# Kernel tuning notes

Hardware: AMD Instinct MI355X
Metric: run time of the kernel (lower is better)

The kernel has to match this reference:

```python
import jax, jax.numpy as jnp
import numpy as np

N = 100000   # nodes
E = 220000   # directed edges (each branch)
H = 128      # hidden_dim
OUT = 1      # output_dim
G = 4096     # num graphs in batch
PE = 5       # laplacian eigenvector PE dims
VOCAB = 28   # atom types


def gcn_conv(x, src, dst, W, b, n):
    # PyG GCNConv: x' = D^-1/2 (A + I) D^-1/2 (X W) + b
    h = x @ W
    deg = jax.ops.segment_sum(jnp.ones(src.shape[0], x.dtype), dst, num_segments=n) + 1.0
    dinv = jax.lax.rsqrt(deg)
    coef = dinv[src] * dinv[dst]                                    # [E]
    agg = jax.ops.segment_sum(h[src] * coef[:, None], dst, num_segments=n)
    agg = agg + h * (dinv * dinv)[:, None]                          # self-loop term
    return agg + b


def gcn2(x, edge_index, W1, b1, W2, b2, n):
    # PyG GCN model, num_layers=2: conv -> relu -> conv
    src, dst = edge_index[0], edge_index[1]
    h = jax.nn.relu(gcn_conv(x, src, dst, W1, b1, n))
    return gcn_conv(h, src, dst, W2, b2, n)


def setup_inputs() -> dict:
    key = jax.random.key(0)
    ks = jax.random.split(key, 16)
    s = 0.1
    return {
        "node_tokens": jax.random.randint(ks[0], (N, 1), 0, VOCAB),
        "pe": jax.random.normal(ks[1], (N, PE), jnp.float32),
        "edge_index": jax.random.randint(ks[2], (2, E), 0, N),
        "vr_edge_index": jax.random.randint(ks[3], (2, E), 0, N),
        "batch": jnp.sort(jax.random.randint(ks[4], (N,), 0, G)),
        "embed_table": jax.random.normal(ks[5], (VOCAB, H), jnp.float32) * s,
        "Wt": jax.random.normal(ks[6], (PE, H), jnp.float32) * s,
        "bt": jnp.zeros((H,), jnp.float32),
        "W1": jax.random.normal(ks[7], (H, H), jnp.float32) * s,
        "b1": jnp.zeros((H,), jnp.float32),
        "W2": jax.random.normal(ks[8], (H, OUT), jnp.float32) * s,
        "b2": jnp.zeros((OUT,), jnp.float32),
        "Wv1": jax.random.normal(ks[9], (H, H), jnp.float32) * s,
        "bv1": jnp.zeros((H,), jnp.float32),
        "Wv2": jax.random.normal(ks[10], (H, OUT), jnp.float32) * s,
        "bv2": jnp.zeros((OUT,), jnp.float32),
    }


def reference(node_tokens, pe, edge_index, vr_edge_index, batch, embed_table,
              Wt, bt, W1, b1, W2, b2, Wv1, bv1, Wv2, bv2):
    # embed_x(data.x.long()).squeeze(1) + lin_trans(pe)
    x = embed_table[node_tokens[:, 0]] + (pe @ Wt + bt)             # [N, H]
    x1 = gcn2(x, edge_index, W1, b1, W2, b2, N)                     # [N, OUT]
    xv = gcn2(x, vr_edge_index, Wv1, bv1, Wv2, bv2, N)              # [N, OUT]
    x1 = x1 + xv
    y_hat = jax.ops.segment_sum(x1, batch, num_segments=G)          # [G, OUT]
    y_hat = jnp.squeeze(y_hat, axis=-1)                             # [G]
    return (y_hat, x)
```

## Files before the change

### kernel.cpp

```cpp
#include <hip/hip_runtime.h>

#define NN 100000
#define NE 220000
#define HD 128
#define NG 4096
#define NPE 5
#define NB_SCAN ((NN + 255) / 256)
#define NBX4 ((NN * HD / 4) / 256)
#define NT16 (NN / 16)
#define NBGEMM 1024
#define NBW 128
#define NBE2 14
#define NBD ((2 * NE + 255) / 256)

typedef unsigned int uint;
typedef unsigned short ushort;
typedef __attribute__((ext_vector_type(8))) short bf16x8;
typedef __attribute__((ext_vector_type(4))) float f32x4;

__device__ __forceinline__ float bf2f(uint u16) {
    return __uint_as_float(u16 << 16);
}
__device__ __forceinline__ ushort f2bf(float f) {
    uint u = __float_as_uint(f);
    u += 0x7fffu + ((u >> 16) & 1u);
    return (ushort)(u >> 16);
}

__global__ void k_prep0(const float* __restrict__ W1, const float* __restrict__ Wv1,
                        const float* __restrict__ embed, const float* __restrict__ bt,
                        ushort* __restrict__ Wcat, float* __restrict__ emb2,
                        const int* __restrict__ ei, const int* __restrict__ vei,
                        int* __restrict__ cnt, int* __restrict__ rank) {
    int b = blockIdx.x;
    if (b < NBW) {
        int t = b * 256 + threadIdx.x;
        int f = t >> 7, k = t & 127;
        const float* W = (f < HD) ? W1 : Wv1;
        Wcat[t] = f2bf(W[k * HD + (f & 127)]);
    } else if (b < NBW + NBE2) {
        int t = (b - NBW) * 256 + threadIdx.x;
        if (t < 28 * 128) emb2[t] = embed[t] + bt[t & 127];
    } else {
        int t = (b - NBW - NBE2) * 256 + threadIdx.x;
        if (t < 2 * NE) {
            int br = t >= NE;
            int e = t - br * NE;
            const int* S = br ? vei : ei;
            rank[t] = atomicAdd(&cnt[br * NN + S[NE + e]], 1);
        }
    }
}

__global__ void k_front_scan1(const int* __restrict__ tok, const float* __restrict__ pe,
                              const float* __restrict__ emb2,
                              const float* __restrict__ Wtr,
                              float* __restrict__ x, ushort* __restrict__ xb,
                              const int* __restrict__ cnt, int* __restrict__ off,
                              int* __restrict__ bsum, float* __restrict__ dinv,
                              float* __restrict__ y) {
    __shared__ int s[256];
    int b = blockIdx.x;
    if (b < 2 * NB_SCAN) {
        int tid = threadIdx.x;
        int gid = b * 256 + tid;
        if (gid < NG) y[gid] = 0.f;
        int br = b / NB_SCAN;
        int blk = b % NB_SCAN;
        int i = blk * 256 + tid;
        int v = (i < NN) ? cnt[br * NN + i] : 0;
        if (i < NN) dinv[br * NN + i] = rsqrtf((float)v + 1.0f);
        s[tid] = v;
        __syncthreads();
        for (int d = 1; d < 256; d <<= 1) {
            int t = (tid >= d) ? s[tid - d] : 0;
            __syncthreads();
            s[tid] += t;
            __syncthreads();
        }
        if (i < NN) off[br * NN + i] = s[tid] - v;
        if (tid == 255) bsum[br * 512 + blk] = s[255];
    } else {
        int idx = (b - 2 * NB_SCAN) * 256 + threadIdx.x;
        int n = idx >> 5, q = idx & 31;
        int t = tok[n];
        float4 acc = ((const float4*)(emb2 + (size_t)t * HD))[q];
        const float* pen = pe + n * NPE;
#pragma unroll
        for (int k = 0; k < NPE; ++k) {
            float p = pen[k];
            float4 wv = ((const float4*)(Wtr + k * HD))[q];
            acc.x += p * wv.x; acc.y += p * wv.y;
            acc.z += p * wv.z; acc.w += p * wv.w;
        }
        ((float4*)x)[idx] = acc;
        uint2 pk;
        pk.x = (uint)f2bf(acc.x) | ((uint)f2bf(acc.y) << 16);
        pk.y = (uint)f2bf(acc.z) | ((uint)f2bf(acc.w) << 16);
        ((uint2*)xb)[idx] = pk;
    }
}

__global__ __launch_bounds__(256) void k_gemm_scan3(
        const ushort* __restrict__ xb, const ushort* __restrict__ Wt,
        ushort* __restrict__ H,
        const int* __restrict__ off, const int* __restrict__ bsum,
        const int* __restrict__ cnt, int2* __restrict__ off2) {
    __shared__ int s[256];
    int b = blockIdx.x;
    if (b < 2 * NB_SCAN) {
        int br = b / NB_SCAN;
        int blk = b % NB_SCAN;
        int tid = threadIdx.x;
        int v = 0;
        if (tid < blk) v = bsum[br * 512 + tid];
        if (tid + 256 < blk) v += bsum[br * 512 + tid + 256];
        s[tid] = v;
#pragma unroll
        for (int d = 128; d > 0; d >>= 1) {
            __syncthreads();
            if (tid < d) s[tid] += s[tid + d];
        }
        __syncthreads();
        int pre = s[0];
        int i = blk * 256 + tid;
        if (i < NN) {
            int o = off[br * NN + i] + pre;
            int2 pr;
            pr.x = o;
            pr.y = o + cnt[br * NN + i];
            off2[br * NN + i] = pr;
        }
    } else {
        int w = threadIdx.x >> 6;
        int lane = threadIdx.x & 63;
        int m = lane & 15, quad = lane >> 4;
        const ushort* Wbase = Wt + ((size_t)(w * 4) * 16 + m) * 128 + quad * 8;
        bf16x8 wf[4][4];
#pragma unroll
        for (int j = 0; j < 4; ++j)
#pragma unroll
            for (int kc = 0; kc < 4; ++kc)
                wf[j][kc] = *(const bf16x8*)(Wbase + (size_t)j * 16 * 128 + kc * 32);

        for (int t = b - 2 * NB_SCAN; t < NT16; t += NBGEMM) {
            int n = t * 16 + m;
            const ushort* Arow = xb + (size_t)n * HD + quad * 8;
            bf16x8 xf[4];
#pragma unroll
            for (int kc = 0; kc < 4; ++kc)
                xf[kc] = *(const bf16x8*)(Arow + kc * 32);
            f32x4 acc[4] = {};
#pragma unroll
            for (int j = 0; j < 4; ++j)
#pragma unroll
                for (int kc = 0; kc < 4; ++kc)
                    acc[j] = __builtin_amdgcn_mfma_f32_16x16x32_bf16(wf[j][kc], xf[kc],
                                                                     acc[j], 0, 0, 0);
#pragma unroll
            for (int j = 0; j < 4; ++j) {
                f32x4 a = acc[j];
                uint2 pk;
                pk.x = (uint)f2bf(a[0]) | ((uint)f2bf(a[1]) << 16);
                pk.y = (uint)f2bf(a[2]) | ((uint)f2bf(a[3]) << 16);
                *(uint2*)&H[(size_t)n * 256 + (w * 4 + j) * 16 + quad * 4] = pk;
            }
        }
    }
}

__global__ void k_scatter(const int* __restrict__ ei, const int* __restrict__ vei,
                          const int* __restrict__ rank, const float* __restrict__ dinv,
                          const int2* __restrict__ off2, int2* __restrict__ ent) {
    int t = blockIdx.x * blockDim.x + threadIdx.x;
    if (t >= 2 * NE) return;
    int br = t >= NE;
    int e = t - br * NE;
    const int* S = br ? vei : ei;
    int s = S[e], d = S[NE + e];
    int pos = off2[br * NN + d].x + rank[t];
    int2 rec;
    rec.x = s;
    rec.y = __float_as_int(dinv[br * NN + s] * dinv[br * NN + d]);
    ent[br * NE + pos] = rec;
}

__global__ void k_gather_ep(const ushort* __restrict__ H, const float* __restrict__ dinv,
                            const int2* __restrict__ off2,
                            const int2* __restrict__ ent,
                            const float* __restrict__ b1, const float* __restrict__ bv1,
                            const float* __restrict__ W2, const float* __restrict__ Wv2,
                            float* __restrict__ z) {
    int wid = threadIdx.x >> 6;
    int lane = threadIdx.x & 63;
    int half = lane >> 5;
    int l = lane & 31;
    int task = blockIdx.x * 8 + wid * 2 + half;
    int br = task >= NN;
    int n = task - br * NN;

    const int2* en = ent + br * NE;
    size_t hoff = (size_t)br * 128;

    int2 pr = off2[br * NN + n];
    int p0 = pr.x, p1 = pr.y;

    float dv = dinv[br * NN + n];
    uint2 u = *(const uint2*)(H + (size_t)n * 256 + hoff + l * 4);
    float c = dv * dv;
    float a0 = bf2f(u.x & 0xffffu) * c, a1 = bf2f(u.x >> 16) * c;
    float a2 = bf2f(u.y & 0xffffu) * c, a3 = bf2f(u.y >> 16) * c;

    for (int p = p0; p < p1; p += 4) {
        int2 e0 = en[p], e1 = en[p + 1], e2 = en[p + 2], e3 = en[p + 3];
        int s0 = e0.x;
        int s1 = (p + 1 < p1) ? e1.x : n;
        int s2 = (p + 2 < p1) ? e2.x : n;
        int s3 = (p + 3 < p1) ? e3.x : n;
        float c0 = __int_as_float(e0.y);
        float c1 = (p + 1 < p1) ? __int_as_float(e1.y) : 0.f;
        float c2 = (p + 2 < p1) ? __int_as_float(e2.y) : 0.f;
        float c3 = (p + 3 < p1) ? __int_as_float(e3.y) : 0.f;
        uint2 v0 = *(const uint2*)(H + (size_t)s0 * 256 + hoff + l * 4);
        uint2 v1 = *(const uint2*)(H + (size_t)s1 * 256 + hoff + l * 4);
        uint2 v2 = *(const uint2*)(H + (size_t)s2 * 256 + hoff + l * 4);
        uint2 v3 = *(const uint2*)(H + (size_t)s3 * 256 + hoff + l * 4);
        a0 += bf2f(v0.x & 0xffffu) * c0; a1 += bf2f(v0.x >> 16) * c0;
        a2 += bf2f(v0.y & 0xffffu) * c0; a3 += bf2f(v0.y >> 16) * c0;
        a0 += bf2f(v1.x & 0xffffu) * c1; a1 += bf2f(v1.x >> 16) * c1;
        a2 += bf2f(v1.y & 0xffffu) * c1; a3 += bf2f(v1.y >> 16) * c1;
        a0 += bf2f(v2.x & 0xffffu) * c2; a1 += bf2f(v2.x >> 16) * c2;
        a2 += bf2f(v2.y & 0xffffu) * c2; a3 += bf2f(v2.y >> 16) * c2;
        a0 += bf2f(v3.x & 0xffffu) * c3; a1 += bf2f(v3.x >> 16) * c3;
        a2 += bf2f(v3.y & 0xffffu) * c3; a3 += bf2f(v3.y >> 16) * c3;
    }

    const float* bb = br ? bv1 : b1;
    const float* ww = br ? Wv2 : W2;
    float4 b4 = *(const float4*)&bb[l * 4];
    float4 w4 = *(const float4*)&ww[l * 4];
    float part = fmaxf(a0 + b4.x, 0.f) * w4.x + fmaxf(a1 + b4.y, 0.f) * w4.y
               + fmaxf(a2 + b4.z, 0.f) * w4.z + fmaxf(a3 + b4.w, 0.f) * w4.w;
#pragma unroll
    for (int o = 16; o > 0; o >>= 1) part += __shfl_down(part, o, 32);
    if (l == 0) z[br * NN + n] = part;
}

__global__ void k_final2(const float* __restrict__ z, const float* __restrict__ dinv,
                         const int2* __restrict__ off2,
                         const int2* __restrict__ ent,
                         const float* __restrict__ b2, const float* __restrict__ bv2,
                         const int* __restrict__ batch, float* __restrict__ y) {
    __shared__ float ybuf[256];
    __shared__ int gbase_s;
    int br = blockIdx.x >= NB_SCAN;
    int nb = blockIdx.x - br * NB_SCAN;
    int tid = threadIdx.x;
    ybuf[tid] = 0.f;
    if (tid == 0) gbase_s = batch[nb * 256];
    __syncthreads();
    int gbase = gbase_s;
    int n = nb * 256 + tid;
    if (n < NN) {
        const int2* en = ent + br * NE;
        float dv = dinv[br * NN + n];
        float acc = z[br * NN + n] * dv * dv;
        int2 pr = off2[br * NN + n];
        int p1 = pr.y;
        for (int p = pr.x; p < p1; p += 4) {
            int2 e0 = en[p], e1 = en[p + 1], e2 = en[p + 2], e3 = en[p + 3];
            int s0 = e0.x;
            int s1 = (p + 1 < p1) ? e1.x : n;
            int s2 = (p + 2 < p1) ? e2.x : n;
            int s3 = (p + 3 < p1) ? e3.x : n;
            float c0 = __int_as_float(e0.y);
            float c1 = (p + 1 < p1) ? __int_as_float(e1.y) : 0.f;
            float c2 = (p + 2 < p1) ? __int_as_float(e2.y) : 0.f;
            float c3 = (p + 3 < p1) ? __int_as_float(e3.y) : 0.f;
            acc += c0 * z[br * NN + s0] + c1 * z[br * NN + s1]
                 + c2 * z[br * NN + s2] + c3 * z[br * NN + s3];
        }
        acc += br ? bv2[0] : b2[0];
        int gi = batch[n] - gbase;
        if (gi < 256) atomicAdd(&ybuf[gi], acc);
        else atomicAdd(&y[batch[n]], acc);
    }
    __syncthreads();
    float v = ybuf[tid];
    if (v != 0.f) atomicAdd(&y[gbase + tid], v);
}

extern "C" void kernel_launch(void* const* d_in, const int* in_sizes, int n_in,
                              void* d_out, int out_size, void* d_ws, size_t ws_size,
                              hipStream_t stream) {
    const int*   tok   = (const int*)d_in[0];
    const float* pe    = (const float*)d_in[1];
    const int*   ei    = (const int*)d_in[2];
    const int*   vei   = (const int*)d_in[3];
    const int*   batch = (const int*)d_in[4];
    const float* embed = (const float*)d_in[5];
    const float* Wtr   = (const float*)d_in[6];
    const float* bt    = (const float*)d_in[7];
    const float* W1    = (const float*)d_in[8];
    const float* b1    = (const float*)d_in[9];
    const float* W2    = (const float*)d_in[10];
    const float* b2    = (const float*)d_in[11];
    const float* Wv1   = (const float*)d_in[12];
    const float* bv1   = (const float*)d_in[13];
    const float* Wv2   = (const float*)d_in[14];
    const float* bv2   = (const float*)d_in[15];

    float* y = (float*)d_out;
    float* x = y + NG;

    char* w = (char*)d_ws;
    ushort* xb   = (ushort*)w;               w += (size_t)NN * HD * 2;
    ushort* H    = (ushort*)w;               w += (size_t)NN * 256 * 2;
    ushort* Wcat = (ushort*)w;               w += 256 * 128 * 2;
    float*  emb2 = (float*)w;                w += 28 * 128 * 4;
    float*  dinv = (float*)w;                w += 2 * NN * 4;
    float*  z    = (float*)w;                w += 2 * NN * 4;
    int*    cnt  = (int*)w;                  w += 2 * NN * 4;
    int*    off  = (int*)w;                  w += 2 * NN * 4;
    int*    rank = (int*)w;                  w += (size_t)2 * NE * 4;
    int2*   off2 = (int2*)w;                 w += (size_t)2 * NN * 8;
    int2*   ent  = (int2*)w;                 w += (size_t)(2 * NE + 8) * 8;
    int*    bsum = (int*)w;                  w += 2 * 512 * 4;

    hipMemsetAsync(cnt, 0, 2 * NN * sizeof(int), stream);

    k_prep0<<<NBW + NBE2 + NBD, 256, 0, stream>>>(W1, Wv1, embed, bt, Wcat, emb2,
                                                  ei, vei, cnt, rank);
    k_front_scan1<<<2 * NB_SCAN + NBX4, 256, 0, stream>>>(tok, pe, emb2, Wtr, x, xb,
                                                          cnt, off, bsum, dinv, y);
    k_gemm_scan3<<<2 * NB_SCAN + NBGEMM, 256, 0, stream>>>(xb, Wcat, H,
                                                           off, bsum, cnt, off2);
    k_scatter<<<NBD, 256, 0, stream>>>(ei, vei, rank, dinv, off2, ent);
    k_gather_ep<<<2 * NN / 8, 256, 0, stream>>>(H, dinv, off2, ent,
                                                b1, bv1, W2, Wv2, z);
    k_final2<<<2 * NB_SCAN, 256, 0, stream>>>(z, dinv, off2, ent,
                                              b2, bv2, batch, y);
}
```

Measured before the change: 222.1 us.

## Add fixed 4-slot per-node edge table to remove dependent offset load in gathers

Adds a padded per-node array that holds the first four incoming edges (source, coefficient) and is filled during the scatter. The gather and final kernels can then load these slots directly, indexed by node id, at the same time as the offset pair, rather than waiting for the CSR offset before fetching edges. The goal is to shorten the dependent-load chain for the typical low-degree node (about 2.2 edges per node). In exchange it enlarges the memset, adds an extra write per edge and 6.4 MB of workspace, and the CSR loop still handles edges beyond the fourth. Empty slots are zeroed, so their coefficient is zero and their index points at node 0.

```diff
diff --git a/kernel.cpp b/kernel.cpp
--- a/kernel.cpp
+++ b/kernel.cpp
@@ -171,23 +171,28 @@
 
 __global__ void k_scatter(const int* __restrict__ ei, const int* __restrict__ vei,
                           const int* __restrict__ rank, const float* __restrict__ dinv,
-                          const int2* __restrict__ off2, int2* __restrict__ ent) {
+                          const int2* __restrict__ off2, int2* __restrict__ ent,
+                          int2* __restrict__ ent8) {
     int t = blockIdx.x * blockDim.x + threadIdx.x;
     if (t >= 2 * NE) return;
     int br = t >= NE;
     int e = t - br * NE;
     const int* S = br ? vei : ei;
     int s = S[e], d = S[NE + e];
-    int pos = off2[br * NN + d].x + rank[t];
+    int rk = rank[t];
+    int base = br * NN + d;
+    int pos = off2[base].x + rk;
     int2 rec;
     rec.x = s;
     rec.y = __float_as_int(dinv[br * NN + s] * dinv[br * NN + d]);
     ent[br * NE + pos] = rec;
+    if (rk < 4) ent8[base * 4 + rk] = rec;
 }
 
 __global__ void k_gather_ep(const ushort* __restrict__ H, const float* __restrict__ dinv,
                             const int2* __restrict__ off2,
                             const int2* __restrict__ ent,
+                            const int4* __restrict__ ent8,
                             const float* __restrict__ b1, const float* __restrict__ bv1,
                             const float* __restrict__ W2, const float* __restrict__ Wv2,
                             float* __restrict__ z) {
@@ -201,17 +206,38 @@
 
     const int2* en = ent + br * NE;
     size_t hoff = (size_t)br * 128;
-
-    int2 pr = off2[br * NN + n];
-    int p0 = pr.x, p1 = pr.y;
-
-    float dv = dinv[br * NN + n];
+    int base = br * NN + n;
+
+    int4 e01 = ent8[base * 2];
+    int4 e23 = ent8[base * 2 + 1];
+    int2 pr = off2[base];
+    float dv = dinv[base];
     uint2 u = *(const uint2*)(H + (size_t)n * 256 + hoff + l * 4);
+
     float c = dv * dv;
     float a0 = bf2f(u.x & 0xffffu) * c, a1 = bf2f(u.x >> 16) * c;
     float a2 = bf2f(u.y & 0xffffu) * c, a3 = bf2f(u.y >> 16) * c;
 
-    for (int p = p0; p < p1; p += 4) {
+    {
+        int s0 = e01.x, s1 = e01.z, s2 = e23.x, s3 = e23.z;
+        float c0 = __int_as_float(e01.y), c1 = __int_as_float(e01.w);
+        float c2 = __int_as_float(e23.y), c3 = __int_as_float(e23.w);
+        uint2 v0 = *(const uint2*)(H + (size_t)s0 * 256 + hoff + l * 4);
+        uint2 v1 = *(const uint2*)(H + (size_t)s1 * 256 + hoff + l * 4);
+        uint2 v2 = *(const uint2*)(H + (size_t)s2 * 256 + hoff + l * 4);
+        uint2 v3 = *(const uint2*)(H + (size_t)s3 * 256 + hoff + l * 4);
+        a0 += bf2f(v0.x & 0xffffu) * c0; a1 += bf2f(v0.x >> 16) * c0;
+        a2 += bf2f(v0.y & 0xffffu) * c0; a3 += bf2f(v0.y >> 16) * c0;
+        a0 += bf2f(v1.x & 0xffffu) * c1; a1 += bf2f(v1.x >> 16) * c1;
+        a2 += bf2f(v1.y & 0xffffu) * c1; a3 += bf2f(v1.y >> 16) * c1;
+        a0 += bf2f(v2.x & 0xffffu) * c2; a1 += bf2f(v2.x >> 16) * c2;
+        a2 += bf2f(v2.y & 0xffffu) * c2; a3 += bf2f(v2.y >> 16) * c2;
+        a0 += bf2f(v3.x & 0xffffu) * c3; a1 += bf2f(v3.x >> 16) * c3;
+        a2 += bf2f(v3.y & 0xffffu) * c3; a3 += bf2f(v3.y >> 16) * c3;
+    }
+
+    int p1 = pr.y;
+    for (int p = pr.x + 4; p < p1; p += 4) {
         int2 e0 = en[p], e1 = en[p + 1], e2 = en[p + 2], e3 = en[p + 3];
         int s0 = e0.x;
         int s1 = (p + 1 < p1) ? e1.x : n;
@@ -249,6 +275,7 @@
 __global__ void k_final2(const float* __restrict__ z, const float* __restrict__ dinv,
                          const int2* __restrict__ off2,
                          const int2* __restrict__ ent,
+                         const int4* __restrict__ ent8,
                          const float* __restrict__ b2, const float* __restrict__ bv2,
                          const int* __restrict__ batch, float* __restrict__ y) {
     __shared__ float ybuf[256];
@@ -263,11 +290,20 @@
     int n = nb * 256 + tid;
     if (n < NN) {
         const int2* en = ent + br * NE;
-        float dv = dinv[br * NN + n];
-        float acc = z[br * NN + n] * dv * dv;
-        int2 pr = off2[br * NN + n];
+        int base = br * NN + n;
+        int4 e01 = ent8[base * 2];
+        int4 e23 = ent8[base * 2 + 1];
+        int2 pr = off2[base];
+        float dv = dinv[base];
+        float acc = z[base] * dv * dv;
+        {
+            float c0 = __int_as_float(e01.y), c1 = __int_as_float(e01.w);
+            float c2 = __int_as_float(e23.y), c3 = __int_as_float(e23.w);
+            acc += c0 * z[br * NN + e01.x] + c1 * z[br * NN + e01.z]
+                 + c2 * z[br * NN + e23.x] + c3 * z[br * NN + e23.z];
+        }
         int p1 = pr.y;
-        for (int p = pr.x; p < p1; p += 4) {
+        for (int p = pr.x + 4; p < p1; p += 4) {
             int2 e0 = en[p], e1 = en[p + 1], e2 = en[p + 2], e3 = en[p + 3];
             int s0 = e0.x;
             int s1 = (p + 1 < p1) ? e1.x : n;
@@ -321,13 +357,14 @@
     float*  dinv = (float*)w;                w += 2 * NN * 4;
     float*  z    = (float*)w;                w += 2 * NN * 4;
     int*    cnt  = (int*)w;                  w += 2 * NN * 4;
+    int2*   ent8 = (int2*)w;                 w += (size_t)2 * NN * 4 * 8;
     int*    off  = (int*)w;                  w += 2 * NN * 4;
     int*    rank = (int*)w;                  w += (size_t)2 * NE * 4;
     int2*   off2 = (int2*)w;                 w += (size_t)2 * NN * 8;
     int2*   ent  = (int2*)w;                 w += (size_t)(2 * NE + 8) * 8;
     int*    bsum = (int*)w;                  w += 2 * 512 * 4;
 
-    hipMemsetAsync(cnt, 0, 2 * NN * sizeof(int), stream);
+    hipMemsetAsync(cnt, 0, (size_t)2 * NN * 4 + (size_t)2 * NN * 4 * 8, stream);
 
     k_prep0<<<NBW + NBE2 + NBD, 256, 0, stream>>>(W1, Wv1, embed, bt, Wcat, emb2,
                                                   ei, vei, cnt, rank);
@@ -335,9 +372,9 @@
                                                           cnt, off, bsum, dinv, y);
     k_gemm_scan3<<<2 * NB_SCAN + NBGEMM, 256, 0, stream>>>(xb, Wcat, H,
                                                            off, bsum, cnt, off2);
-    k_scatter<<<NBD, 256, 0, stream>>>(ei, vei, rank, dinv, off2, ent);
-    k_gather_ep<<<2 * NN / 8, 256, 0, stream>>>(H, dinv, off2, ent,
+    k_scatter<<<NBD, 256, 0, stream>>>(ei, vei, rank, dinv, off2, ent, ent8);
+    k_gather_ep<<<2 * NN / 8, 256, 0, stream>>>(H, dinv, off2, ent, (const int4*)ent8,
                                                 b1, bv1, W2, Wv2, z);
-    k_final2<<<2 * NB_SCAN, 256, 0, stream>>>(z, dinv, off2, ent,
+    k_final2<<<2 * NB_SCAN, 256, 0, stream>>>(z, dinv, off2, ent, (const int4*)ent8,
                                               b2, bv2, batch, y);
 }
```

After: 228.7 us. +3.0%, slower.
